# Kernel optimization log

Hardware: AMD Instinct MI355X
Metric: run time of the kernel (lower is better)

## Reference

```python
import jax, jax.numpy as jnp
import numpy as np
from jax import lax

_K1 = np.array([[0,0,0,0,0],[0,-1,2,-1,0],[0,2,4,2,0],[0,-1,2,-1,0],[0,0,0,0,0]], dtype=np.float32)
_K2 = np.array([[-1,2,-2,2,-1],[2,-6,8,-6,2],[-2,8,-12,8,-2],[2,-6,8,-6,2],[-1,2,-2,2,-1]], dtype=np.float32)
_K3 = np.array([[0,0,0,0,0],[0,0,0,0,0],[0,1,-2,1,0],[0,0,0,0,0],[0,0,0,0,0]], dtype=np.float32)

def _depthwise_filter(k, C):
    # OIHW with feature_group_count=C -> (C, 1, 5, 5)
    return jnp.broadcast_to(jnp.asarray(k)[None, None], (C, 1, 5, 5))

def _dwconv(x, f):
    C = x.shape[1]
    return lax.conv_general_dilated(
        x, f, window_strides=(1, 1), padding=[(2, 2), (2, 2)],
        dimension_numbers=('NCHW', 'OIHW', 'NCHW'), feature_group_count=C)

def setup_inputs() -> dict:
    key = jax.random.key(0)
    x = jax.random.normal(key, (64, 3, 512, 512), dtype=jnp.float32)
    return {"x": x}

def reference(x):
    C = x.shape[1]
    f1 = _depthwise_filter(_K1, C)
    f2 = _depthwise_filter(_K2, C)
    f3 = _depthwise_filter(_K3, C)
    edge = _dwconv(x, f1)
    texture = _dwconv(edge, f2)
    residual = _dwconv(texture, f3)
    return residual
```

## Files before the change

### kernel.cpp

```cpp
#include <hip/hip_runtime.h>


#define H 512
#define W 512
#define RS 32
#define STRIPS (H/RS)

__device__ __forceinline__ void load_row(const float* __restrict__ xp, int gr, int cb,
                                         int lane, float v[8], float& vl, float& vh) {
    if (gr >= 0 && gr < H) {
        const float4* p = (const float4*)(xp + gr * W + cb);
        float4 a = p[0], b = p[1];
        v[0] = a.x; v[1] = a.y; v[2] = a.z; v[3] = a.w;
        v[4] = b.x; v[5] = b.y; v[6] = b.z; v[7] = b.w;
    } else {
        #pragma unroll
        for (int j = 0; j < 8; ++j) v[j] = 0.f;
    }
    vl = __shfl_up(v[7], 1, 64);
    vh = __shfl_down(v[0], 1, 64);
    if (lane == 0)  vl = 0.f;
    if (lane == 63) vh = 0.f;
}

__global__ __launch_bounds__(256, 3)
void resid_kernel(const float* __restrict__ x, float* __restrict__ out) {
    const int lane  = threadIdx.x & 63;
    const int wid   = (blockIdx.x << 2) | (threadIdx.x >> 6);
    const int plane = wid >> 4;
    const int strip = wid & (STRIPS - 1);
    const int r0    = strip * RS;
    const int cb    = lane << 3;

    const float* __restrict__ xp = x + (size_t)plane * (H * W);
    float* __restrict__ op = out + (size_t)plane * (H * W);

    float xa[8], xb[8], xc[8];
    float xal, xah, xbl, xbh, xcl, xch;
    float Lw[5][8], Mw[3][8];

    #pragma unroll
    for (int k = 0; k < 5; ++k)
        #pragma unroll
        for (int j = 0; j < 8; ++j) Lw[k][j] = 0.f;
    #pragma unroll
    for (int k = 0; k < 3; ++k)
        #pragma unroll
        for (int j = 0; j < 8; ++j) Mw[k][j] = 0.f;

    load_row(xp, r0 - 3, cb, lane, xa, xal, xah);
    load_row(xp, r0 - 2, cb, lane, xb, xbl, xbh);

    for (int er = r0 - 2; er <= r0 + RS + 1; ++er) {
        load_row(xp, er + 1, cb, lane, xc, xcl, xch);

        float Lr[8], Mr[8];
        if (er >= 0 && er < H) {
            float s[8], e[8];
            #pragma unroll
            for (int j = 0; j < 8; ++j) s[j] = xa[j] + xc[j];
            float sl = xal + xcl, sh = xah + xch;
            #pragma unroll
            for (int j = 0; j < 8; ++j) {
                float sm = ((j == 0) ? sl  : s[j-1]) + ((j == 7) ? sh  : s[j+1]);
                float xm = ((j == 0) ? xbl : xb[j-1]) + ((j == 7) ? xbh : xb[j+1]);
                e[j] = 2.f*s[j] - sm + 2.f*xm + 4.f*xb[j];
            }
            float el1 = __shfl_up(e[7], 1, 64);
            float el2 = __shfl_up(e[6], 1, 64);
            float eh1 = __shfl_down(e[0], 1, 64);
            float eh2 = __shfl_down(e[1], 1, 64);
            if (lane == 0)  { el1 = 0.f; el2 = 0.f; }
            if (lane == 63) { eh1 = 0.f; eh2 = 0.f; }
            #pragma unroll
            for (int j = 0; j < 8; ++j) {
                float em1 = (j == 0) ? el1 : e[j-1];
                float ep1 = (j == 7) ? eh1 : e[j+1];
                float em2 = (j == 0) ? el2 : ((j == 1) ? el1 : e[j-2]);
                float ep2 = (j == 7) ? eh2 : ((j == 6) ? eh1 : e[j+2]);
                float pj = em1 + ep1;
                float qj = em2 + ep2;
                Lr[j] = qj - 2.f*pj + 2.f*e[j];
                Mr[j] = pj - 2.f*e[j];
            }
        } else {
            #pragma unroll
            for (int j = 0; j < 8; ++j) { Lr[j] = 0.f; Mr[j] = 0.f; }
        }

        #pragma unroll
        for (int j = 0; j < 8; ++j) {
            Lw[0][j] = Lw[1][j]; Lw[1][j] = Lw[2][j];
            Lw[2][j] = Lw[3][j]; Lw[3][j] = Lw[4][j];
            Lw[4][j] = Lr[j];
        }

        if (er >= r0 + 2) {
            const int orow = er - 2;
            float t[8];
            #pragma unroll
            for (int j = 0; j < 8; ++j) {
                float lsum = Lw[0][j] - 2.f*Lw[1][j] + 2.f*Lw[2][j] - 2.f*Lw[3][j] + Lw[4][j];
                float msum = Mw[0][j] - 2.f*Mw[1][j] + Mw[2][j];
                t[j] = -lsum - 2.f*msum;
            }
            float tl = __shfl_up(t[7], 1, 64);
            float th = __shfl_down(t[0], 1, 64);
            if (lane == 0)  tl = 0.f;
            if (lane == 63) th = 0.f;
            float r[8];
            #pragma unroll
            for (int j = 0; j < 8; ++j) {
                float rm = (j == 0) ? tl : t[j-1];
                float rp = (j == 7) ? th : t[j+1];
                r[j] = rm + rp - 2.f*t[j];
            }
            float4 o0 = make_float4(r[0], r[1], r[2], r[3]);
            float4 o1 = make_float4(r[4], r[5], r[6], r[7]);
            float* dst = op + orow * W + cb;
            *(float4*)(dst)     = o0;
            *(float4*)(dst + 4) = o1;
        }

        #pragma unroll
        for (int j = 0; j < 8; ++j) {
            Mw[0][j] = Mw[1][j]; Mw[1][j] = Mw[2][j]; Mw[2][j] = Mr[j];
        }
        #pragma unroll
        for (int j = 0; j < 8; ++j) { xa[j] = xb[j]; xb[j] = xc[j]; }
        xal = xbl; xah = xbh; xbl = xcl; xbh = xch;
    }
}

extern "C" void kernel_launch(void* const* d_in, const int* in_sizes, int n_in,
                              void* d_out, int out_size, void* d_ws, size_t ws_size,
                              hipStream_t stream) {
    const float* x = (const float*)d_in[0];
    float* out = (float*)d_out;
    resid_kernel<<<dim3(768), dim3(256), 0, stream>>>(x, out);
}
```

Baseline: 360.7 us.

## Prefetch rows two iterations ahead, halve strip height, use nontemporal stores

Input rows are now issued two iterations before use (through the P/Q registers), so the global load latency overlaps with the stencil math. Strips drop to 16 rows and the grid doubles to 1536 blocks, with a higher occupancy hint in launch bounds, to expose more parallelism. Output writes become nontemporal stores to avoid polluting the cache. In exchange, halo recomputation per strip grows relative to useful rows, and the extra prefetch registers push against the tighter register budget.

Result: slower. 1.127 ms (+212.3%).

```diff
diff --git a/kernel.cpp b/kernel.cpp
--- a/kernel.cpp
+++ b/kernel.cpp
@@ -3,33 +3,39 @@
 
 #define H 512
 #define W 512
-#define RS 32
+#define RS 16
 #define STRIPS (H/RS)
 
-__device__ __forceinline__ void load_row(const float* __restrict__ xp, int gr, int cb,
-                                         int lane, float v[8], float& vl, float& vh) {
-    if (gr >= 0 && gr < H) {
-        const float4* p = (const float4*)(xp + gr * W + cb);
-        float4 a = p[0], b = p[1];
+typedef float vf4 __attribute__((ext_vector_type(4)));
+
+__device__ __forceinline__ void issue_load(const float* __restrict__ xp, int gr, int rmax,
+                                           int cb, float v[8]) {
+    if (gr >= 0 && gr < H && gr <= rmax) {
+        const vf4* p = (const vf4*)(xp + gr * W + cb);
+        vf4 a = p[0], b = p[1];
         v[0] = a.x; v[1] = a.y; v[2] = a.z; v[3] = a.w;
         v[4] = b.x; v[5] = b.y; v[6] = b.z; v[7] = b.w;
     } else {
         #pragma unroll
         for (int j = 0; j < 8; ++j) v[j] = 0.f;
     }
+}
+
+__device__ __forceinline__ void halo(int lane, const float v[8], float& vl, float& vh) {
     vl = __shfl_up(v[7], 1, 64);
     vh = __shfl_down(v[0], 1, 64);
     if (lane == 0)  vl = 0.f;
     if (lane == 63) vh = 0.f;
 }
 
-__global__ __launch_bounds__(256, 3)
+__global__ __launch_bounds__(256, 5)
 void resid_kernel(const float* __restrict__ x, float* __restrict__ out) {
     const int lane  = threadIdx.x & 63;
     const int wid   = (blockIdx.x << 2) | (threadIdx.x >> 6);
-    const int plane = wid >> 4;
+    const int plane = wid >> 5;
     const int strip = wid & (STRIPS - 1);
     const int r0    = strip * RS;
+    const int rmax  = r0 + RS + 2;
     const int cb    = lane << 3;
 
     const float* __restrict__ xp = x + (size_t)plane * (H * W);
@@ -37,6 +43,7 @@
 
     float xa[8], xb[8], xc[8];
     float xal, xah, xbl, xbh, xcl, xch;
+    float P[8], Q[8];
     float Lw[5][8], Mw[3][8];
 
     #pragma unroll
@@ -48,11 +55,16 @@
         #pragma unroll
         for (int j = 0; j < 8; ++j) Mw[k][j] = 0.f;
 
-    load_row(xp, r0 - 3, cb, lane, xa, xal, xah);
-    load_row(xp, r0 - 2, cb, lane, xb, xbl, xbh);
+    issue_load(xp, r0 - 3, rmax, cb, xa);
+    issue_load(xp, r0 - 2, rmax, cb, xb);
+    issue_load(xp, r0 - 1, rmax, cb, xc);
+    issue_load(xp, r0,     rmax, cb, P);
+    halo(lane, xa, xal, xah);
+    halo(lane, xb, xbl, xbh);
+    halo(lane, xc, xcl, xch);
 
     for (int er = r0 - 2; er <= r0 + RS + 1; ++er) {
-        load_row(xp, er + 1, cb, lane, xc, xcl, xch);
+        issue_load(xp, er + 3, rmax, cb, Q);
 
         float Lr[8], Mr[8];
         if (er >= 0 && er < H) {
@@ -115,11 +127,11 @@
                 float rp = (j == 7) ? th : t[j+1];
                 r[j] = rm + rp - 2.f*t[j];
             }
-            float4 o0 = make_float4(r[0], r[1], r[2], r[3]);
-            float4 o1 = make_float4(r[4], r[5], r[6], r[7]);
             float* dst = op + orow * W + cb;
-            *(float4*)(dst)     = o0;
-            *(float4*)(dst + 4) = o1;
+            vf4 o0 = { r[0], r[1], r[2], r[3] };
+            vf4 o1 = { r[4], r[5], r[6], r[7] };
+            __builtin_nontemporal_store(o0, (vf4*)dst);
+            __builtin_nontemporal_store(o1, (vf4*)(dst + 4));
         }
 
         #pragma unroll
@@ -127,8 +139,11 @@
             Mw[0][j] = Mw[1][j]; Mw[1][j] = Mw[2][j]; Mw[2][j] = Mr[j];
         }
         #pragma unroll
-        for (int j = 0; j < 8; ++j) { xa[j] = xb[j]; xb[j] = xc[j]; }
+        for (int j = 0; j < 8; ++j) { xa[j] = xb[j]; xb[j] = xc[j]; xc[j] = P[j]; }
         xal = xbl; xah = xbh; xbl = xcl; xbh = xch;
+        halo(lane, xc, xcl, xch);
+        #pragma unroll
+        for (int j = 0; j < 8; ++j) P[j] = Q[j];
     }
 }
 
@@ -137,5 +152,5 @@
                               hipStream_t stream) {
     const float* x = (const float*)d_in[0];
     float* out = (float*)d_out;
-    resid_kernel<<<dim3(768), dim3(256), 0, stream>>>(x, out);
+    resid_kernel<<<dim3(1536), dim3(256), 0, stream>>>(x, out);
 }
```
